# Kernel tuning notes

Measured on AMD Instinct MI355X. Metric: run time of the kernel, lower is better.

The kernel has to match this reference:

```python
import jax, jax.numpy as jnp
import numpy as np

EPS = 1e-5

def _branch(x, W, gamma, beta):
    # 1x1 conv (no bias) + InstanceNorm2d(affine) + ReLU
    y = jnp.einsum('oc,bchw->bohw', W, x)
    mu = y.mean(axis=(2, 3), keepdims=True)
    var = y.var(axis=(2, 3), keepdims=True)
    y = (y - mu) * jax.lax.rsqrt(var + EPS)
    y = y * gamma[None, :, None, None] + beta[None, :, None, None]
    return jax.nn.relu(y)

def setup_inputs() -> dict:
    key = jax.random.key(0)
    ks = jax.random.split(key, 12)
    b, in_ch, h, w = 2, 256, 64, 64
    c = in_ch // 8
    d = dict(
        x1=jax.random.normal(ks[0], (b, in_ch, h, w), jnp.float32),
        x2=jax.random.normal(ks[1], (b, in_ch, h, w), jnp.float32),
        x3=jax.random.normal(ks[2], (b, in_ch, h, w), jnp.float32),
        W1=jax.random.normal(ks[3], (c, in_ch), jnp.float32) * (1.0 / np.sqrt(in_ch)),
        g1=jnp.ones((c,), jnp.float32), b1=jnp.zeros((c,), jnp.float32),
        W2=jax.random.normal(ks[4], (c, in_ch), jnp.float32) * (1.0 / np.sqrt(in_ch)),
        g2=jnp.ones((c,), jnp.float32), b2=jnp.zeros((c,), jnp.float32),
        W3=jax.random.normal(ks[5], (c, in_ch), jnp.float32) * (1.0 / np.sqrt(in_ch)),
        g3=jnp.ones((c,), jnp.float32), b3=jnp.zeros((c,), jnp.float32),
    )
    return d

def _forward(x1, x2, x3, W1, g1, b1, W2, g2, b2, W3, g3, b3):
    q1 = _branch(x1, W1, g1, b1); q2 = _branch(x2, W1, g1, b1); q3 = _branch(x3, W1, g1, b1)
    k1 = _branch(x1, W2, g2, b2); k2 = _branch(x2, W2, g2, b2); k3 = _branch(x3, W2, g2, b2)
    v1 = _branch(x1, W3, g3, b3); v2 = _branch(x2, W3, g3, b3); v3 = _branch(x3, W3, g3, b3)
    b_, c, h, w = q1.shape
    hw = h * w
    Q1 = q1.reshape(b_, c, hw).transpose(0, 2, 1)  # [b,hw,c]
    Q2 = q2.reshape(b_, c, hw).transpose(0, 2, 1)
    Q3 = q3.reshape(b_, c, hw).transpose(0, 2, 1)
    K1 = k1.reshape(b_, c, hw)                      # [b,c,hw]
    K2 = k2.reshape(b_, c, hw)
    K3 = k3.reshape(b_, c, hw)
    sm = lambda Q, K: jax.nn.softmax(jnp.einsum('bic,bcj->bij', Q, K), axis=-1)
    A12 = sm(Q1, K2); A21 = sm(Q2, K1); A23 = sm(Q2, K3)
    A32 = sm(Q3, K2); A13 = sm(Q1, K3)
    # ones[b,c,hw] @ A == broadcast of column-sums of A: track a [b,hw] vector
    colsum = lambda A: A.sum(axis=1)                        # [b,hw]
    step = lambda v, A: jnp.einsum('bk,bkj->bj', v, A)      # [b,hw]
    def bc(v):  # broadcast [b,hw] -> [b,c,h,w]
        return jnp.broadcast_to(v[:, None, :], (b_, c, hw)).reshape(b_, c, h, w)
    p1a = bc(step(step(step(colsum(A12), A23), A32), A21))
    p1b = bc(step(colsum(A12), A21))
    p2 = bc(step(colsum(A23), A32))
    p3a = bc(step(colsum(A12), A23))
    p3b = bc(colsum(A13))
    return (p1a, p1b, p2, p3a, p3b, v1, v2, v3)

def reference(x1, x2, x3, W1, g1, b1, W2, g2, b2, W3, g3, b3):
    return _forward(x1, x2, x3, W1, g1, b1, W2, g2, b2, W3, g3, b3)
```

## Files before the change

### kernel.cpp

```cpp
#include <hip/hip_runtime.h>

typedef unsigned short u16;
typedef u16  u16x8  __attribute__((ext_vector_type(8)));
typedef _Float16 f16x4 __attribute__((ext_vector_type(4)));
typedef _Float16 f16x8 __attribute__((ext_vector_type(8)));
typedef float f32x2 __attribute__((ext_vector_type(2)));
typedef float f32x4 __attribute__((ext_vector_type(4)));

#define HW 4096
#define CIN 256
#define HW32 (HW * 32)
#define L2E 1.4426950408889634f

__device__ __forceinline__ float fexp2(float x) { return __builtin_amdgcn_exp2f(x); }

__global__ __launch_bounds__(256) void convert_kernel(const float* x1, const float* x2, const float* x3,
        const float* W1, const float* W2, const float* W3,
        _Float16* xh, _Float16* wh, float* mean, float* maxq, float* maxk) {
    int bx = blockIdx.x; int t = threadIdx.x;
    if (bx < 1536) {
        int xi = bx >> 9, b = (bx >> 8) & 1, c = bx & 255;
        const float* src = (xi == 0 ? x1 : xi == 1 ? x2 : x3) + (size_t)(b * CIN + c) * HW;
        _Float16* dst = xh + ((size_t)((xi * 2 + b) * CIN) + c) * HW;
        float s = 0.f;
        for (int i = t; i < 1024; i += 256) {
            f32x4 v = ((const f32x4*)src)[i];
            s += v[0] + v[1] + v[2] + v[3];
            f16x4 h;
#pragma unroll
            for (int r = 0; r < 4; ++r) h[r] = (_Float16)v[r];
            ((f16x4*)dst)[i] = h;
        }
        __shared__ float red[256];
        red[t] = s; __syncthreads();
        for (int k = 128; k; k >>= 1) { if (t < k) red[t] += red[t + k]; __syncthreads(); }
        if (t == 0) mean[(xi * 2 + b) * CIN + c] = red[0] * (1.f / HW);
    } else {
        int j = bx - 1536;
        if (j == 0 && t < 12) { if (t < 6) maxq[t] = 0.f; else maxk[t - 6] = 0.f; }
        int widx = j >> 1, half = j & 1;
        const float* wsrc = (widx == 0 ? W1 : widx == 1 ? W2 : W3) + half * 4096;
        _Float16* wdst = wh + widx * 8192 + half * 4096;
        for (int i = t; i < 1024; i += 256) {
            f32x4 v = ((const f32x4*)wsrc)[i];
            f16x4 h;
#pragma unroll
            for (int r = 0; r < 4; ++r) h[r] = (_Float16)v[r];
            ((f16x4*)wdst)[i] = h;
        }
    }
}

__global__ __launch_bounds__(256) void m2_kernel(const _Float16* xh, float* Pm2) {
    int xi = blockIdx.y, b = blockIdx.z;
    int xb = xi * 2 + b;
    const _Float16* X = xh + (size_t)xb * CIN * HW;
    int bx = blockIdx.x;
    int chunk = bx >> 4, blk = bx & 15;
    int t = threadIdx.x; int wv = t >> 6; int L = t & 63; int m = L & 15; int quad = L >> 4;
    int region = blk * 4 + wv;
    int r1 = (region >> 3) * 32, r2 = (region & 7) * 32;
    int p0 = chunk * 512 + quad * 8;
    const f16x8* A0 = (const f16x8*)(X + (size_t)(r1 + m) * HW + p0);
    const f16x8* A1 = (const f16x8*)(X + (size_t)(r1 + 16 + m) * HW + p0);
    const f16x8* B0 = (const f16x8*)(X + (size_t)(r2 + m) * HW + p0);
    const f16x8* B1 = (const f16x8*)(X + (size_t)(r2 + 16 + m) * HW + p0);
    f32x4 zero = {0, 0, 0, 0};
    f32x4 acc00 = zero, acc01 = zero, acc10 = zero, acc11 = zero;
#pragma unroll 4
    for (int it = 0; it < 16; ++it) {
        f16x8 a0 = A0[it * 4], a1 = A1[it * 4];
        f16x8 b0 = B0[it * 4], b1 = B1[it * 4];
        acc00 = __builtin_amdgcn_mfma_f32_16x16x32_f16(a0, b0, acc00, 0, 0, 0);
        acc01 = __builtin_amdgcn_mfma_f32_16x16x32_f16(a0, b1, acc01, 0, 0, 0);
        acc10 = __builtin_amdgcn_mfma_f32_16x16x32_f16(a1, b0, acc10, 0, 0, 0);
        acc11 = __builtin_amdgcn_mfma_f32_16x16x32_f16(a1, b1, acc11, 0, 0, 0);
    }
    float* dst = Pm2 + ((size_t)chunk * 6 + xb) * 65536;
#pragma unroll
    for (int r = 0; r < 4; ++r) {
        int row0 = (r1 + quad * 4 + r) * 256, row1 = (r1 + 16 + quad * 4 + r) * 256;
        dst[row0 + r2 + m] = acc00[r];
        dst[row0 + r2 + 16 + m] = acc01[r];
        dst[row1 + r2 + m] = acc10[r];
        dst[row1 + r2 + 16 + m] = acc11[r];
    }
}

__global__ __launch_bounds__(256) void m2combine_kernel(const float* Pm2, float* M2) {
    size_t e = (size_t)blockIdx.x * 256 + threadIdx.x;
    float s = 0.f;
#pragma unroll
    for (int c = 0; c < 8; ++c) s += Pm2[(size_t)c * 6 * 65536 + e];
    M2[e] = s * (1.f / HW);
}

__global__ __launch_bounds__(256) void stats_kernel(const float* M2, const float* mean,
        const float* W1, const float* W2, const float* W3,
        const float* g1, const float* g2, const float* g3,
        const float* b1, const float* b2, const float* b3, float2* afine) {
    int o = blockIdx.x; int xi = blockIdx.y; int b = blockIdx.z;
    int widx = o >> 5; int oc = o & 31;
    const float* Wp = (widx == 0 ? W1 : widx == 1 ? W2 : W3) + oc * CIN;
    const float* gp = (widx == 0 ? g1 : widx == 1 ? g2 : g3);
    const float* bp = (widx == 0 ? b1 : widx == 1 ? b2 : b3);
    int t = threadIdx.x;
    __shared__ float sW[256];
    __shared__ float red[256];
    sW[t] = Wp[t];
    __syncthreads();
    const float* m2row = M2 + ((size_t)(xi * 2 + b) * CIN + t) * CIN;
    float tv = 0.f;
    const f32x4* r4 = (const f32x4*)m2row;
#pragma unroll 4
    for (int k = 0; k < 64; ++k) {
        f32x4 mv = r4[k];
        const f32x4 wv = *(const f32x4*)&sW[k * 4];
        tv += mv[0] * wv[0] + mv[1] * wv[1] + mv[2] * wv[2] + mv[3] * wv[3];
    }
    red[t] = tv * sW[t]; __syncthreads();
    for (int k = 128; k; k >>= 1) { if (t < k) red[t] += red[t + k]; __syncthreads(); }
    float E2 = red[0]; __syncthreads();
    red[t] = sW[t] * mean[(xi * 2 + b) * CIN + t]; __syncthreads();
    for (int k = 128; k; k >>= 1) { if (t < k) red[t] += red[t + k]; __syncthreads(); }
    if (t == 0) {
        float mu = red[0];
        float var = E2 - mu * mu;
        float rsig = rsqrtf(var + 1e-5f);
        float scale = gp[oc] * rsig;
        float bias = bp[oc] - mu * scale;
        if (widx == 0) { scale *= L2E; bias *= L2E; }
        afine[(xi * 2 + b) * 96 + o] = make_float2(scale, bias);
    }
}

__global__ __launch_bounds__(256) void conv_kernel(const _Float16* xh, const _Float16* wh,
        const float2* afine, _Float16* qT, _Float16* kT, float* out,
        float* maxq, float* maxk) {
    int xi = blockIdx.y, b = blockIdx.z;
    const u16* xb = (const u16*)(xh + (size_t)(xi * 2 + b) * CIN * HW);
    int p0 = blockIdx.x * 64;
    __shared__ u16 lds[32 * 65 * 8];
    __shared__ float smq[4], smk[4];
    int t = threadIdx.x;
    {
        int pc = t & 7, cg = t >> 3;
        u16x8 a[8];
#pragma unroll
        for (int r = 0; r < 8; ++r)
            a[r] = *(const u16x8*)(xb + (size_t)(cg * 8 + r) * HW + p0 + pc * 8);
#pragma unroll
        for (int i = 0; i < 8; ++i) {
            u16x8 d;
#pragma unroll
            for (int r = 0; r < 8; ++r) d[r] = a[r][i];
            int p = pc * 8 + i; int fp = p ^ (p >> 3);
            *(u16x8*)&lds[(cg * 65 + fp) * 8] = d;
        }
    }
    __syncthreads();
    int wv = t >> 6, L = t & 63, m = L & 15, quad = L >> 4;
    int pw0 = wv * 16;
    f16x8 af[8];
    {
        int p = pw0 + m; int fp = p ^ (p >> 3);
#pragma unroll
        for (int k = 0; k < 8; ++k)
            af[k] = *(const f16x8*)&lds[((k * 4 + quad) * 65 + fp) * 8];
    }
    int xb2 = xi * 2 + b;
    float sqq[4] = {0, 0, 0, 0}, sqk[4] = {0, 0, 0, 0};
    for (int ot = 0; ot < 6; ++ot) {
        int o0 = ot * 16; int widx = ot >> 1;
        int o_col = o0 + m;
        f32x4 acc = {0, 0, 0, 0};
#pragma unroll
        for (int k = 0; k < 8; ++k) {
            f16x8 bfr = *(const f16x8*)(wh + (size_t)o_col * CIN + k * 32 + quad * 8);
            acc = __builtin_amdgcn_mfma_f32_16x16x32_f16(af[k], bfr, acc, 0, 0, 0);
        }
        float2 afv = afine[xb2 * 96 + o_col];
        f32x4 vals;
#pragma unroll
        for (int r = 0; r < 4; ++r) {
            float v = acc[r] * afv.x + afv.y;
            vals[r] = v > 0.f ? v : 0.f;
        }
        int prow = p0 + pw0 + quad * 4;
        if (widx < 2) {
            _Float16* dst = (widx == 0 ? qT : kT) + (size_t)xb2 * HW32;
            int cc = (o0 & 31) + m;
#pragma unroll
            for (int r = 0; r < 4; ++r)
                dst[(size_t)(prow + r) * 32 + cc] = (_Float16)vals[r];
            if (widx == 0) {
#pragma unroll
                for (int r = 0; r < 4; ++r) sqq[r] += vals[r] * vals[r];
            } else {
#pragma unroll
                for (int r = 0; r < 4; ++r) sqk[r] += vals[r] * vals[r];
            }
        } else {
            float* dst = out + (size_t)(5 + xi) * 262144 + (size_t)b * 131072 + (size_t)(o_col - 64) * HW + prow;
            *(f32x4*)dst = vals;
        }
    }
#pragma unroll
    for (int msk = 1; msk <= 8; msk <<= 1) {
#pragma unroll
        for (int r = 0; r < 4; ++r) {
            sqq[r] += __shfl_xor(sqq[r], msk);
            sqk[r] += __shfl_xor(sqk[r], msk);
        }
    }
    float nq = fmaxf(fmaxf(sqq[0], sqq[1]), fmaxf(sqq[2], sqq[3]));
    float nk = fmaxf(fmaxf(sqk[0], sqk[1]), fmaxf(sqk[2], sqk[3]));
    nq = fmaxf(nq, __shfl_xor(nq, 16)); nq = fmaxf(nq, __shfl_xor(nq, 32));
    nk = fmaxf(nk, __shfl_xor(nk, 16)); nk = fmaxf(nk, __shfl_xor(nk, 32));
    if (L == 0) { smq[wv] = nq; smk[wv] = nk; }
    __syncthreads();
    if (t == 0) {
        float bq = fmaxf(fmaxf(smq[0], smq[1]), fmaxf(smq[2], smq[3]));
        float bk = fmaxf(fmaxf(smk[0], smk[1]), fmaxf(smk[2], smk[3]));
        atomicMax((unsigned*)&maxq[xb2], __float_as_uint(bq));
        atomicMax((unsigned*)&maxk[xb2], __float_as_uint(bk));
    }
}

__global__ __launch_bounds__(256) void zsweep_kernel(const _Float16* qT, const _Float16* kT,
        const float* maxq, const float* maxk, float* Pz) {
    const int qxA[5] = {0, 1, 1, 2, 0};
    const int kxA[5] = {1, 0, 2, 1, 2};
    int mat = blockIdx.y, b = blockIdx.z;
    const _Float16* qb = qT + (size_t)(qxA[mat] * 2 + b) * HW32;
    const _Float16* kb = kT + (size_t)(kxA[mat] * 2 + b) * HW32;
    float Cg = sqrtf(maxq[qxA[mat] * 2 + b]) * sqrtf(maxk[kxA[mat] * 2 + b]);
    int bx = blockIdx.x;
    int jc = bx & 15, qblk = bx >> 4;
    int t = threadIdx.x; int wv = t >> 6; int L = t & 63; int m = L & 15; int quad = L >> 4;
    int i0 = qblk * 256 + wv * 64;
    f16x8 a[4];
#pragma unroll
    for (int tt = 0; tt < 4; ++tt)
        a[tt] = *(const f16x8*)(qb + (size_t)(i0 + tt * 16 + m) * 32 + quad * 8);
    const f16x8* kp = (const f16x8*)(kb + m * 32 + quad * 8) + (size_t)jc * (16 * 64);
    f32x4 negC = {-Cg, -Cg, -Cg, -Cg};
    f32x4 zero = {0.f, 0.f, 0.f, 0.f};
    f32x4 z[4] = {zero, zero, zero, zero};
#pragma unroll 4
    for (int j = 0; j < 16; ++j) {
        f16x8 bf = kp[j * 64];
#pragma unroll
        for (int tt = 0; tt < 4; ++tt) {
            f32x4 d = __builtin_amdgcn_mfma_f32_16x16x32_f16(a[tt], bf, negC, 0, 0, 0);
            f32x4 e = {fexp2(d[0]), fexp2(d[1]), fexp2(d[2]), fexp2(d[3])};
            z[tt] = z[tt] + e;
        }
    }
#pragma unroll
    for (int tt = 0; tt < 4; ++tt)
#pragma unroll
        for (int msk = 1; msk <= 8; msk <<= 1) {
            z[tt][0] += __shfl_xor(z[tt][0], msk); z[tt][1] += __shfl_xor(z[tt][1], msk);
            z[tt][2] += __shfl_xor(z[tt][2], msk); z[tt][3] += __shfl_xor(z[tt][3], msk);
        }
    if (m == 0) {
        int mb = mat * 2 + b;
#pragma unroll
        for (int tt = 0; tt < 4; ++tt) {
            int row = i0 + tt * 16 + quad * 4;
#pragma unroll
            for (int r = 0; r < 4; ++r)
                Pz[((size_t)mb * 16 + jc) * HW + row + r] = z[tt][r];
        }
    }
}

__global__ __launch_bounds__(256) void zcombine_kernel(const float* Pz, float* R, float2* Wa) {
    int mb = blockIdx.y;
    int r = blockIdx.x * 256 + threadIdx.x;
    float Z = 0.f;
#pragma unroll
    for (int c = 0; c < 16; ++c) Z += Pz[((size_t)mb * 16 + c) * HW + r];
    float rz = 1.0f / Z;
    size_t idx = (size_t)mb * HW + r;
    R[idx] = rz;
    if (mb < 2 || mb >= 8) Wa[idx] = make_float2(rz, 0.f);
}

struct PCfg {
    const _Float16* qb; const _Float16* kb;
    const float* mq; const float* mk;
    const float2* wt;
    float2* Pp;
    int nit;
    int dual;
};

__global__ __launch_bounds__(256) void pass2p_kernel(PCfg c0, PCfg c1) {
    PCfg c = (blockIdx.y == 0) ? c0 : c1;
    int b = blockIdx.z;
    int bx = blockIdx.x; int jb = bx & 15; int ic = bx >> 4;
    const _Float16* qb = c.qb + (size_t)b * HW32;
    const _Float16* kb = c.kb + (size_t)b * HW32;
    const f32x2* wt = (const f32x2*)(c.wt + (size_t)b * HW);
    float Cg = sqrtf(c.mq[b]) * sqrtf(c.mk[b]);
    int t = threadIdx.x; int wv = t >> 6; int L = t & 63; int m = L & 15; int quad = L >> 4;
    int j0 = jb * 256 + wv * 64;
    f16x8 bf[4];
#pragma unroll
    for (int tt = 0; tt < 4; ++tt)
        bf[tt] = *(const f16x8*)(kb + (size_t)(j0 + tt * 16 + m) * 32 + quad * 8);
    f32x4 negC = {-Cg, -Cg, -Cg, -Cg};
    f32x2 acc[4] = {{0, 0}, {0, 0}, {0, 0}, {0, 0}};
    int ibase = ic * (c.nit * 16);
    if (c.dual) {
#pragma unroll 4
        for (int it = 0; it < c.nit; ++it) {
            int i0 = ibase + it * 16;
            f16x8 av = *(const f16x8*)(qb + (size_t)(i0 + m) * 32 + quad * 8);
            const f32x2* wr = wt + i0 + quad * 4;
            f32x2 w0 = wr[0], w1 = wr[1], w2 = wr[2], w3 = wr[3];
#pragma unroll
            for (int tt = 0; tt < 4; ++tt) {
                f32x4 d = __builtin_amdgcn_mfma_f32_16x16x32_f16(av, bf[tt], negC, 0, 0, 0);
                float e0 = fexp2(d[0]), e1 = fexp2(d[1]), e2 = fexp2(d[2]), e3 = fexp2(d[3]);
                acc[tt] += (f32x2){e0, e0} * w0;
                acc[tt] += (f32x2){e1, e1} * w1;
                acc[tt] += (f32x2){e2, e2} * w2;
                acc[tt] += (f32x2){e3, e3} * w3;
            }
        }
    } else {
#pragma unroll 4
        for (int it = 0; it < c.nit; ++it) {
            int i0 = ibase + it * 16;
            f16x8 av = *(const f16x8*)(qb + (size_t)(i0 + m) * 32 + quad * 8);
            const f32x2* wr = wt + i0 + quad * 4;
            float w0 = wr[0][0], w1 = wr[1][0], w2 = wr[2][0], w3 = wr[3][0];
#pragma unroll
            for (int tt = 0; tt < 4; ++tt) {
                f32x4 d = __builtin_amdgcn_mfma_f32_16x16x32_f16(av, bf[tt], negC, 0, 0, 0);
                float e0 = fexp2(d[0]), e1 = fexp2(d[1]), e2 = fexp2(d[2]), e3 = fexp2(d[3]);
                acc[tt][0] += e0 * w0 + e1 * w1 + e2 * w2 + e3 * w3;
            }
        }
    }
#pragma unroll
    for (int tt = 0; tt < 4; ++tt) {
        acc[tt][0] += __shfl_xor(acc[tt][0], 16); acc[tt][0] += __shfl_xor(acc[tt][0], 32);
        acc[tt][1] += __shfl_xor(acc[tt][1], 16); acc[tt][1] += __shfl_xor(acc[tt][1], 32);
    }
    if (quad == 0) {
        float2* dst = c.Pp + ((size_t)ic * 2 + b) * HW;
#pragma unroll
        for (int tt = 0; tt < 4; ++tt)
            dst[j0 + tt * 16 + m] = make_float2(acc[tt][0], acc[tt][1]);
    }
}

__global__ __launch_bounds__(256) void prepA_kernel(const float2* PpA, const float* R,
        float* c12, float* c13, float2* Wa2) {
    int b = blockIdx.y; int j = blockIdx.x * 256 + threadIdx.x;
    float s12 = 0.f, s13 = 0.f;
    for (int ic = 0; ic < 16; ++ic) {
        s12 += PpA[((size_t)ic * 2 + b) * HW + j].x;
        s13 += PpA[((size_t)(16 + ic) * 2 + b) * HW + j].x;
    }
    c12[(size_t)b * HW + j] = s12; c13[(size_t)b * HW + j] = s13;
    float rn = R[((size_t)(2 * 2 + b)) * HW + j];
    Wa2[(size_t)b * HW + j] = make_float2(rn, s12 * rn);
}

__global__ __launch_bounds__(256) void prep_kernel(const float2* Pp, const float* Rn,
        const float* aux, float* o1, float* o2, float2* Wn, int IC, int mode) {
    int b = blockIdx.y; int j = blockIdx.x * 256 + threadIdx.x;
    float s1 = 0.f, s2 = 0.f;
    for (int ic = 0; ic < IC; ++ic) {
        float2 p = Pp[((size_t)ic * 2 + b) * HW + j];
        s1 += p.x; s2 += p.y;
    }
    if (o1) o1[(size_t)b * HW + j] = s1;
    if (o2) o2[(size_t)b * HW + j] = s2;
    if (Wn) {
        float rn = Rn[(size_t)b * HW + j];
        float2 w = (mode == 0) ? make_float2(s1 * rn, s2 * rn)
                               : make_float2(s2 * rn, aux[(size_t)b * HW + j] * rn);
        Wn[(size_t)b * HW + j] = w;
    }
}

__global__ __launch_bounds__(256) void bcast_kernel(const float* vecs, float* out) {
    int bx = blockIdx.x;
    int s = bx >> 6; int rem = bx & 63; int b = rem >> 5; int c = rem & 31;
    const float* src = vecs + ((size_t)s * 2 + b) * HW;
    float* dst = out + ((size_t)(s * 2 + b) * 32 + c) * HW;
    int t = threadIdx.x;
#pragma unroll
    for (int k = 0; k < 4; ++k)
        ((f32x4*)dst)[k * 256 + t] = ((const f32x4*)src)[k * 256 + t];
}

extern "C" void kernel_launch(void* const* d_in, const int* in_sizes, int n_in,
                              void* d_out, int out_size, void* d_ws, size_t ws_size,
                              hipStream_t stream) {
    (void)in_sizes; (void)n_in; (void)out_size; (void)ws_size;
    const float* x1 = (const float*)d_in[0];
    const float* x2 = (const float*)d_in[1];
    const float* x3 = (const float*)d_in[2];
    const float* W1 = (const float*)d_in[3];
    const float* g1 = (const float*)d_in[4];
    const float* b1 = (const float*)d_in[5];
    const float* W2 = (const float*)d_in[6];
    const float* g2 = (const float*)d_in[7];
    const float* b2 = (const float*)d_in[8];
    const float* W3 = (const float*)d_in[9];
    const float* g3 = (const float*)d_in[10];
    const float* b3 = (const float*)d_in[11];
    float* out = (float*)d_out;

    char* w = (char*)d_ws;
    _Float16* xh    = (_Float16*)(w);
    _Float16* wh    = (_Float16*)(w + 12582912);
    float*    mean  = (float*)(w + 12632064);
    float*    M2    = (float*)(w + 12638208);
    float2*   afine = (float2*)(w + 14211072);
    _Float16* qT    = (_Float16*)(w + 14215680);
    _Float16* kT    = (_Float16*)(w + 15788544);
    float*    R     = (float*)(w + 17361408);
    float*    maxq  = (float*)(w + 17525248);
    float*    maxk  = (float*)(w + 17525312);
    float2*   Wa    = (float2*)(w + 17689088);
    float*    vecs  = (float*)(w + 18016768);
    float*    Pz    = (float*)(w + 18213376);
    float2*   PpA   = (float2*)(w + 23456256);
    float2*   PpB   = (float2*)(w + 25553408);
    float2*   PpC   = (float2*)(w + 27650560);
    float2*   PpD   = (float2*)(w + 29747712);
    float*    Pm2   = (float*)(w + 18213376);

    float* v_p1a = vecs + 0 * 2 * HW;
    float* v_p1b = vecs + 1 * 2 * HW;
    float* v_p2  = vecs + 2 * 2 * HW;
    float* v_p3a = vecs + 3 * 2 * HW;
    float* v_p3b = vecs + 4 * 2 * HW;
    float* v_c12 = vecs + 5 * 2 * HW;

    hipLaunchKernelGGL(convert_kernel, dim3(1542), dim3(256), 0, stream,
                       x1, x2, x3, W1, W2, W3, xh, wh, mean, maxq, maxk);
    hipLaunchKernelGGL(m2_kernel, dim3(128, 3, 2), dim3(256), 0, stream, xh, Pm2);
    hipLaunchKernelGGL(m2combine_kernel, dim3(1536), dim3(256), 0, stream, Pm2, M2);
    hipLaunchKernelGGL(stats_kernel, dim3(96, 3, 2), dim3(256), 0, stream,
                       M2, mean, W1, W2, W3, g1, g2, g3, b1, b2, b3, afine);
    hipLaunchKernelGGL(conv_kernel, dim3(64, 3, 2), dim3(256), 0, stream,
                       xh, wh, afine, qT, kT, out, maxq, maxk);
    hipLaunchKernelGGL(zsweep_kernel, dim3(256, 5, 2), dim3(256), 0, stream, qT, kT, maxq, maxk, Pz);
    hipLaunchKernelGGL(zcombine_kernel, dim3(16, 10), dim3(256), 0, stream, Pz, R, Wa);

    PCfg cA0 = { qT + 0 * 2 * HW32, kT + 1 * 2 * HW32, maxq + 0, maxk + 2, Wa + 0 * 2 * HW, PpA,               16, 0 };
    PCfg cA1 = { qT + 0 * 2 * HW32, kT + 2 * 2 * HW32, maxq + 0, maxk + 4, Wa + 4 * 2 * HW, PpA + 16 * 2 * HW, 16, 0 };
    hipLaunchKernelGGL(pass2p_kernel, dim3(256, 2, 2), dim3(256), 0, stream, cA0, cA1);
    hipLaunchKernelGGL(prepA_kernel, dim3(16, 2), dim3(256), 0, stream,
                       PpA, R, v_c12, v_p3b, Wa + 2 * 2 * HW);

    PCfg cB = { qT + 1 * 2 * HW32, kT + 2 * 2 * HW32, maxq + 2, maxk + 4, Wa + 2 * 2 * HW, PpB, 8, 1 };
    hipLaunchKernelGGL(pass2p_kernel, dim3(512, 1, 2), dim3(256), 0, stream, cB, cB);
    hipLaunchKernelGGL(prep_kernel, dim3(16, 2), dim3(256), 0, stream,
                       PpB, R + 3 * 2 * HW, (const float*)nullptr,
                       (float*)nullptr, v_p3a, Wa + 3 * 2 * HW, 32, 0);

    PCfg cC = { qT + 2 * 2 * HW32, kT + 1 * 2 * HW32, maxq + 4, maxk + 2, Wa + 3 * 2 * HW, PpC, 8, 1 };
    hipLaunchKernelGGL(pass2p_kernel, dim3(512, 1, 2), dim3(256), 0, stream, cC, cC);
    hipLaunchKernelGGL(prep_kernel, dim3(16, 2), dim3(256), 0, stream,
                       PpC, R + 1 * 2 * HW, v_c12,
                       v_p2, (float*)nullptr, Wa + 1 * 2 * HW, 32, 1);

    PCfg cD = { qT + 1 * 2 * HW32, kT + 0 * 2 * HW32, maxq + 2, maxk + 0, Wa + 1 * 2 * HW, PpD, 8, 1 };
    hipLaunchKernelGGL(pass2p_kernel, dim3(512, 1, 2), dim3(256), 0, stream, cD, cD);
    hipLaunchKernelGGL(prep_kernel, dim3(16, 2), dim3(256), 0, stream,
                       PpD, (const float*)nullptr, (const float*)nullptr,
                       v_p1a, v_p1b, (float2*)nullptr, 32, 0);

    hipLaunchKernelGGL(bcast_kernel, dim3(320), dim3(256), 0, stream, vecs, out);
}
```

Baseline: 263.2 us.

## Fuse softmax normalizer and partial-sum reduction into pass2 and broadcast kernels

Removes the zcombine, prepA and prep kernels. Each pass2p block now reduces the Pz partials and previous-stage partial sums for its own row slice into shared memory before the MFMA loop. The final broadcast kernel reduces the partial buffers directly while writing the output. This cuts five kernel launches and the intermediate R/Wa/vecs round trips. In exchange, every column block redundantly recomputes the same row reductions (16 or 32 loads per row), which adds global reads and a sync before the main loop.

```diff
diff --git a/kernel.cpp b/kernel.cpp
--- a/kernel.cpp
+++ b/kernel.cpp
@@ -276,25 +276,15 @@
     }
 }
 
-__global__ __launch_bounds__(256) void zcombine_kernel(const float* Pz, float* R, float2* Wa) {
-    int mb = blockIdx.y;
-    int r = blockIdx.x * 256 + threadIdx.x;
-    float Z = 0.f;
-#pragma unroll
-    for (int c = 0; c < 16; ++c) Z += Pz[((size_t)mb * 16 + c) * HW + r];
-    float rz = 1.0f / Z;
-    size_t idx = (size_t)mb * HW + r;
-    R[idx] = rz;
-    if (mb < 2 || mb >= 8) Wa[idx] = make_float2(rz, 0.f);
-}
-
 struct PCfg {
     const _Float16* qb; const _Float16* kb;
     const float* mq; const float* mk;
-    const float2* wt;
+    const float* PzR;
+    const float2* w1src;
+    const float2* w2src;
     float2* Pp;
     int nit;
-    int dual;
+    int ic1, comp1, ic2, comp2;
 };
 
 __global__ __launch_bounds__(256) void pass2p_kernel(PCfg c0, PCfg c1) {
@@ -303,9 +293,40 @@
     int bx = blockIdx.x; int jb = bx & 15; int ic = bx >> 4;
     const _Float16* qb = c.qb + (size_t)b * HW32;
     const _Float16* kb = c.kb + (size_t)b * HW32;
-    const f32x2* wt = (const f32x2*)(c.wt + (size_t)b * HW);
     float Cg = sqrtf(c.mq[b]) * sqrtf(c.mk[b]);
     int t = threadIdx.x; int wv = t >> 6; int L = t & 63; int m = L & 15; int quad = L >> 4;
+    int ibase = ic * (c.nit * 16);
+    int rows = c.nit * 16;
+    __shared__ float2 wlds[256];
+    {
+        for (int r = t; r < rows; r += 256) {
+            int i = ibase + r;
+            const float* pz = c.PzR + (size_t)b * (16 * HW) + i;
+            float Z = 0.f;
+#pragma unroll
+            for (int cc = 0; cc < 16; ++cc) Z += pz[cc * HW];
+            float rz = 1.0f / Z;
+            float wx, wy = 0.f;
+            if (c.w1src) {
+                float s = 0.f;
+                for (int cc = 0; cc < c.ic1; ++cc) {
+                    float2 p = c.w1src[((size_t)cc * 2 + b) * HW + i];
+                    s += c.comp1 ? p.y : p.x;
+                }
+                wx = s * rz;
+            } else wx = rz;
+            if (c.w2src) {
+                float s = 0.f;
+                for (int cc = 0; cc < c.ic2; ++cc) {
+                    float2 p = c.w2src[((size_t)cc * 2 + b) * HW + i];
+                    s += c.comp2 ? p.y : p.x;
+                }
+                wy = s * rz;
+            }
+            wlds[r] = make_float2(wx, wy);
+        }
+    }
+    __syncthreads();
     int j0 = jb * 256 + wv * 64;
     f16x8 bf[4];
 #pragma unroll
@@ -313,14 +334,15 @@
         bf[tt] = *(const f16x8*)(kb + (size_t)(j0 + tt * 16 + m) * 32 + quad * 8);
     f32x4 negC = {-Cg, -Cg, -Cg, -Cg};
     f32x2 acc[4] = {{0, 0}, {0, 0}, {0, 0}, {0, 0}};
-    int ibase = ic * (c.nit * 16);
-    if (c.dual) {
+    int dual = (c.w2src != nullptr);
+    if (dual) {
 #pragma unroll 4
         for (int it = 0; it < c.nit; ++it) {
             int i0 = ibase + it * 16;
             f16x8 av = *(const f16x8*)(qb + (size_t)(i0 + m) * 32 + quad * 8);
-            const f32x2* wr = wt + i0 + quad * 4;
-            f32x2 w0 = wr[0], w1 = wr[1], w2 = wr[2], w3 = wr[3];
+            const float2* wr = &wlds[it * 16 + quad * 4];
+            f32x2 w0 = {wr[0].x, wr[0].y}, w1 = {wr[1].x, wr[1].y};
+            f32x2 w2 = {wr[2].x, wr[2].y}, w3 = {wr[3].x, wr[3].y};
 #pragma unroll
             for (int tt = 0; tt < 4; ++tt) {
                 f32x4 d = __builtin_amdgcn_mfma_f32_16x16x32_f16(av, bf[tt], negC, 0, 0, 0);
@@ -336,8 +358,8 @@
         for (int it = 0; it < c.nit; ++it) {
             int i0 = ibase + it * 16;
             f16x8 av = *(const f16x8*)(qb + (size_t)(i0 + m) * 32 + quad * 8);
-            const f32x2* wr = wt + i0 + quad * 4;
-            float w0 = wr[0][0], w1 = wr[1][0], w2 = wr[2][0], w3 = wr[3][0];
+            const float2* wr = &wlds[it * 16 + quad * 4];
+            float w0 = wr[0].x, w1 = wr[1].x, w2 = wr[2].x, w3 = wr[3].x;
 #pragma unroll
             for (int tt = 0; tt < 4; ++tt) {
                 f32x4 d = __builtin_amdgcn_mfma_f32_16x16x32_f16(av, bf[tt], negC, 0, 0, 0);
@@ -359,46 +381,20 @@
     }
 }
 
-__global__ __launch_bounds__(256) void prepA_kernel(const float2* PpA, const float* R,
-        float* c12, float* c13, float2* Wa2) {
-    int b = blockIdx.y; int j = blockIdx.x * 256 + threadIdx.x;
-    float s12 = 0.f, s13 = 0.f;
-    for (int ic = 0; ic < 16; ++ic) {
-        s12 += PpA[((size_t)ic * 2 + b) * HW + j].x;
-        s13 += PpA[((size_t)(16 + ic) * 2 + b) * HW + j].x;
-    }
-    c12[(size_t)b * HW + j] = s12; c13[(size_t)b * HW + j] = s13;
-    float rn = R[((size_t)(2 * 2 + b)) * HW + j];
-    Wa2[(size_t)b * HW + j] = make_float2(rn, s12 * rn);
-}
-
-__global__ __launch_bounds__(256) void prep_kernel(const float2* Pp, const float* Rn,
-        const float* aux, float* o1, float* o2, float2* Wn, int IC, int mode) {
-    int b = blockIdx.y; int j = blockIdx.x * 256 + threadIdx.x;
-    float s1 = 0.f, s2 = 0.f;
-    for (int ic = 0; ic < IC; ++ic) {
-        float2 p = Pp[((size_t)ic * 2 + b) * HW + j];
-        s1 += p.x; s2 += p.y;
-    }
-    if (o1) o1[(size_t)b * HW + j] = s1;
-    if (o2) o2[(size_t)b * HW + j] = s2;
-    if (Wn) {
-        float rn = Rn[(size_t)b * HW + j];
-        float2 w = (mode == 0) ? make_float2(s1 * rn, s2 * rn)
-                               : make_float2(s2 * rn, aux[(size_t)b * HW + j] * rn);
-        Wn[(size_t)b * HW + j] = w;
-    }
-}
-
-__global__ __launch_bounds__(256) void bcast_kernel(const float* vecs, float* out) {
+__global__ __launch_bounds__(256) void bcast_kernel(const float2* PpA2, const float2* PpB,
+        const float2* PpC, const float2* PpD, float* out) {
     int bx = blockIdx.x;
-    int s = bx >> 6; int rem = bx & 63; int b = rem >> 5; int c = rem & 31;
-    const float* src = vecs + ((size_t)s * 2 + b) * HW;
-    float* dst = out + ((size_t)(s * 2 + b) * 32 + c) * HW;
-    int t = threadIdx.x;
-#pragma unroll
-    for (int k = 0; k < 4; ++k)
-        ((f32x4*)dst)[k * 256 + t] = ((const f32x4*)src)[k * 256 + t];
+    int sb = bx >> 4; int s = sb >> 1; int b = sb & 1; int js = bx & 15;
+    int j = js * 256 + threadIdx.x;
+    float v = 0.f;
+    if (s == 0)      { for (int ic = 0; ic < 32; ++ic) v += PpD[((size_t)ic * 2 + b) * HW + j].x; }
+    else if (s == 1) { for (int ic = 0; ic < 32; ++ic) v += PpD[((size_t)ic * 2 + b) * HW + j].y; }
+    else if (s == 2) { for (int ic = 0; ic < 32; ++ic) v += PpC[((size_t)ic * 2 + b) * HW + j].x; }
+    else if (s == 3) { for (int ic = 0; ic < 32; ++ic) v += PpB[((size_t)ic * 2 + b) * HW + j].y; }
+    else             { for (int ic = 0; ic < 16; ++ic) v += PpA2[((size_t)ic * 2 + b) * HW + j].x; }
+    float* dst = out + ((size_t)(s * 2 + b) * 32) * HW + j;
+#pragma unroll
+    for (int c = 0; c < 32; ++c) dst[(size_t)c * HW] = v;
 }
 
 extern "C" void kernel_launch(void* const* d_in, const int* in_sizes, int n_in,
@@ -427,24 +423,15 @@
     float2*   afine = (float2*)(w + 14211072);
     _Float16* qT    = (_Float16*)(w + 14215680);
     _Float16* kT    = (_Float16*)(w + 15788544);
-    float*    R     = (float*)(w + 17361408);
     float*    maxq  = (float*)(w + 17525248);
     float*    maxk  = (float*)(w + 17525312);
-    float2*   Wa    = (float2*)(w + 17689088);
-    float*    vecs  = (float*)(w + 18016768);
     float*    Pz    = (float*)(w + 18213376);
     float2*   PpA   = (float2*)(w + 23456256);
     float2*   PpB   = (float2*)(w + 25553408);
     float2*   PpC   = (float2*)(w + 27650560);
     float2*   PpD   = (float2*)(w + 29747712);
     float*    Pm2   = (float*)(w + 18213376);
-
-    float* v_p1a = vecs + 0 * 2 * HW;
-    float* v_p1b = vecs + 1 * 2 * HW;
-    float* v_p2  = vecs + 2 * 2 * HW;
-    float* v_p3a = vecs + 3 * 2 * HW;
-    float* v_p3b = vecs + 4 * 2 * HW;
-    float* v_c12 = vecs + 5 * 2 * HW;
+    float2*   PpA2  = PpA + 16 * 2 * HW;
 
     hipLaunchKernelGGL(convert_kernel, dim3(1542), dim3(256), 0, stream,
                        x1, x2, x3, W1, W2, W3, xh, wh, mean, maxq, maxk);
@@ -455,31 +442,24 @@
     hipLaunchKernelGGL(conv_kernel, dim3(64, 3, 2), dim3(256), 0, stream,
                        xh, wh, afine, qT, kT, out, maxq, maxk);
     hipLaunchKernelGGL(zsweep_kernel, dim3(256, 5, 2), dim3(256), 0, stream, qT, kT, maxq, maxk, Pz);
-    hipLaunchKernelGGL(zcombine_kernel, dim3(16, 10), dim3(256), 0, stream, Pz, R, Wa);
-
-    PCfg cA0 = { qT + 0 * 2 * HW32, kT + 1 * 2 * HW32, maxq + 0, maxk + 2, Wa + 0 * 2 * HW, PpA,               16, 0 };
-    PCfg cA1 = { qT + 0 * 2 * HW32, kT + 2 * 2 * HW32, maxq + 0, maxk + 4, Wa + 4 * 2 * HW, PpA + 16 * 2 * HW, 16, 0 };
+
+    PCfg cA0 = { qT + 0 * 2 * HW32, kT + 1 * 2 * HW32, maxq + 0, maxk + 2,
+                 Pz + (size_t)0 * 32 * HW, nullptr, nullptr, PpA,  16, 0, 0, 0, 0 };
+    PCfg cA1 = { qT + 0 * 2 * HW32, kT + 2 * 2 * HW32, maxq + 0, maxk + 4,
+                 Pz + (size_t)4 * 32 * HW, nullptr, nullptr, PpA2, 16, 0, 0, 0, 0 };
     hipLaunchKernelGGL(pass2p_kernel, dim3(256, 2, 2), dim3(256), 0, stream, cA0, cA1);
-    hipLaunchKernelGGL(prepA_kernel, dim3(16, 2), dim3(256), 0, stream,
-                       PpA, R, v_c12, v_p3b, Wa + 2 * 2 * HW);
-
-    PCfg cB = { qT + 1 * 2 * HW32, kT + 2 * 2 * HW32, maxq + 2, maxk + 4, Wa + 2 * 2 * HW, PpB, 8, 1 };
+
+    PCfg cB = { qT + 1 * 2 * HW32, kT + 2 * 2 * HW32, maxq + 2, maxk + 4,
+                Pz + (size_t)2 * 32 * HW, nullptr, PpA, PpB, 8, 0, 0, 16, 0 };
     hipLaunchKernelGGL(pass2p_kernel, dim3(512, 1, 2), dim3(256), 0, stream, cB, cB);
-    hipLaunchKernelGGL(prep_kernel, dim3(16, 2), dim3(256), 0, stream,
-                       PpB, R + 3 * 2 * HW, (const float*)nullptr,
-                       (float*)nullptr, v_p3a, Wa + 3 * 2 * HW, 32, 0);
-
-    PCfg cC = { qT + 2 * 2 * HW32, kT + 1 * 2 * HW32, maxq + 4, maxk + 2, Wa + 3 * 2 * HW, PpC, 8, 1 };
+
+    PCfg cC = { qT + 2 * 2 * HW32, kT + 1 * 2 * HW32, maxq + 4, maxk + 2,
+                Pz + (size_t)3 * 32 * HW, PpB, PpB, PpC, 8, 32, 0, 32, 1 };
     hipLaunchKernelGGL(pass2p_kernel, dim3(512, 1, 2), dim3(256), 0, stream, cC, cC);
-    hipLaunchKernelGGL(prep_kernel, dim3(16, 2), dim3(256), 0, stream,
-                       PpC, R + 1 * 2 * HW, v_c12,
-                       v_p2, (float*)nullptr, Wa + 1 * 2 * HW, 32, 1);
-
-    PCfg cD = { qT + 1 * 2 * HW32, kT + 0 * 2 * HW32, maxq + 2, maxk + 0, Wa + 1 * 2 * HW, PpD, 8, 1 };
+
+    PCfg cD = { qT + 1 * 2 * HW32, kT + 0 * 2 * HW32, maxq + 2, maxk + 0,
+                Pz + (size_t)1 * 32 * HW, PpC, PpA, PpD, 8, 32, 1, 16, 0 };
     hipLaunchKernelGGL(pass2p_kernel, dim3(512, 1, 2), dim3(256), 0, stream, cD, cD);
-    hipLaunchKernelGGL(prep_kernel, dim3(16, 2), dim3(256), 0, stream,
-                       PpD, (const float*)nullptr, (const float*)nullptr,
-                       v_p1a, v_p1b, (float2*)nullptr, 32, 0);
-
-    hipLaunchKernelGGL(bcast_kernel, dim3(320), dim3(256), 0, stream, vecs, out);
-}
+
+    hipLaunchKernelGGL(bcast_kernel, dim3(160), dim3(256), 0, stream, PpA2, PpB, PpC, PpD, out);
+}
```

Measured after the change: 264.6 us. No clear change (+0.5%).
